# Kernel tuning notes

Hardware: AMD Instinct MI355X
Metric: run time of the kernel (lower is better)

## Reference

```python
import jax, jax.numpy as jnp
import numpy as np

K = 3          # kernel_size (forced by hardcoded padding=1 in query unfold)
PAD = 1        # padding
C_IN = 64      # conv in_channels (x has C_IN + 5 channels)
C_OUT = 128    # out_channels
B, H, W = 16, 32, 32


def unfold(x, k, pad=0, mode='constant'):
    """torch.nn.functional.unfold equivalent. x: (B,C,H,W) -> (B, C*k*k, L).
    Ordering matches torch: channel slowest, then kernel row, then kernel col."""
    if pad:
        x = jnp.pad(x, ((0, 0), (0, 0), (pad, pad), (pad, pad)), mode=mode)
    b, c, h, w = x.shape
    oh, ow = h - k + 1, w - k + 1
    # (B, C, k*k, oh, ow) with patch index i*k+j
    patches = jnp.stack([x[:, :, i:i + oh, j:j + ow]
                         for i in range(k) for j in range(k)], axis=2)
    return patches.reshape(b, c * k * k, oh * ow)


def conv2d(x, w, b, pad):
    out = jax.lax.conv_general_dilated(
        x, w, window_strides=(1, 1), padding=[(pad, pad), (pad, pad)],
        dimension_numbers=('NCHW', 'OIHW', 'NCHW'))
    return out + b[None, :, None, None]


def setup_inputs() -> dict:
    key = jax.random.key(0)
    ks = jax.random.split(key, 6)
    fan1 = C_IN * K * K
    fan2 = C_OUT * 1 * 1
    return {
        'x': jax.random.normal(ks[0], (B, C_IN + 5, H, W), jnp.float32),
        'conv_w': jax.random.normal(ks[1], (C_OUT, C_IN, K, K), jnp.float32) / np.sqrt(fan1),
        'conv_b': jax.random.normal(ks[2], (C_OUT,), jnp.float32) * 0.01,
        'conv2_w': jax.random.normal(ks[3], (1, C_OUT, 1, 1), jnp.float32) / np.sqrt(fan2),
        'conv2_b': jax.random.normal(ks[4], (1,), jnp.float32) * 0.01,
        'shapes_kernel': jax.random.uniform(ks[5], (1, C_OUT, K * K * 5, 1), jnp.float32),
    }


def reference(x, conv_w, conv_b, conv2_w, conv2_b, shapes_kernel):
    k, pad = K, PAD
    center = k * k // 2

    conv_out = conv2d(x[:, :-5], conv_w, conv_b, pad)          # (B, C_OUT, H', W')
    b, cout, oh, ow = conv_out.shape
    L = oh * ow

    # shape-channel windows (replication-padded), center-relative positions
    sw = unfold(x[:, -5:], k, pad, 'edge').reshape(b, 5, k * k, L)
    sw = sw.at[:, 0:2].add(-sw[:, 0:2, center:center + 1])

    # L1 distance of each window to each learned shape kernel
    sd = jnp.abs(sw.reshape(b, 1, 5 * k * k, L) - shapes_kernel).sum(axis=2)  # (B, C_OUT, L)
    sd = sd.reshape(b, cout, oh, ow)

    saf = jax.nn.relu(conv_out / (sd + 1.0))                    # shape_attended_features

    q = conv2d(saf, conv2_w, conv2_b, 0) / jnp.sqrt(jnp.float32(cout))  # (B, 1, H', W')
    qu = jax.nn.softmax(unfold(q, k, 1), axis=1)[:, None]       # (B, 1, k*k, L), zero-padded

    u_mean = unfold(x[:, -5:-3], k, pad, 'edge').reshape(b, 2, k * k, L)
    means = (u_mean * qu).sum(axis=2)                           # (B, 2, L)

    v1 = (unfold(x[:, -3:-1], k, pad, 'edge').reshape(b, 2, k * k, L) * qu).sum(axis=2)
    v2 = (((u_mean - means[:, :, None, :]) ** 2) * qu).sum(axis=2)
    var = v1 + v2                                               # (B, 2, L)

    c1 = (unfold(x[:, -1:], k, pad, 'edge').reshape(b, 1, k * k, L) * qu).sum(axis=2)
    c2 = ((u_mean[:, 0:1] - means[:, 0:1, None, :]) *
          (u_mean[:, 1:2] - means[:, 1:2, None, :]) * qu).sum(axis=2)
    covar = c1 + c2                                             # (B, 1, L)

    agg = jnp.concatenate([means, var, covar], axis=1).reshape(b, 5, oh, ow)
    return jnp.concatenate([saf, agg], axis=1)                  # (B, C_OUT+5, H', W')
```

## Files before the change

### kernel.cpp

```cpp
#include <hip/hip_runtime.h>
#include <math.h>

#define CI 64
#define CO 128
#define CX 69
#define LPIX 1024

typedef __attribute__((ext_vector_type(8))) short bf16x8;
typedef __attribute__((ext_vector_type(4))) float f32x4;

#define WMF_OFF  0
#define SKT_OFF  147456
#define QP_OFF   (147456 + 23040)

__device__ __forceinline__ unsigned short f2bf(float f) {
  unsigned u = __float_as_uint(f);
  unsigned r = (u + 0x7fffu + ((u >> 16) & 1u)) >> 16;
  return (unsigned short)r;
}

__launch_bounds__(256)
__global__ void prepW(const float* __restrict__ cwg,
                      const float* __restrict__ skg,
                      unsigned short* __restrict__ wmf,
                      float* __restrict__ skt) {
  int i = blockIdx.x * 256 + threadIdx.x;
  if (i < 128 * 9 * 64) {
    int co = i / 576, rem = i - co * 576;
    int tap = rem >> 6, ci = rem & 63;
    wmf[i] = f2bf(cwg[co * 576 + ci * 9 + tap]);
  } else {
    int d = i - 128 * 9 * 64;
    if (d < 45 * 128) {
      int j = d >> 7, co = d & 127;
      skt[j * 128 + co] = skg[co * 45 + j];
    }
  }
}

__launch_bounds__(256, 2)
__global__ void convFused(const float* __restrict__ xg,
                          const unsigned short* __restrict__ wmfg,
                          const float* __restrict__ cbg,
                          const float* __restrict__ w2g,
                          const float* __restrict__ sktg,
                          float* __restrict__ qp,
                          float* __restrict__ outg) {
  __shared__ char arena[18432];
  __shared__ float lds_sx[5 * 144];
  __shared__ float qred[4][64];

  unsigned short* ldsB = (unsigned short*)arena;
  float* lds_c = (float*)arena;

  const int tid = threadIdx.x;
  const int blk = blockIdx.x;
  const int coh = blk & 1;
  const int rp  = (blk >> 1) & 15;
  const int b   = blk >> 5;
  const int r0  = rp * 2;

  const int w    = tid >> 6;
  const int lane = tid & 63;
  const int rsel = w >> 1;
  const int cq   = w & 1;
  const int n16  = lane & 15;
  const int kq   = lane >> 4;

  const float* xb = xg + (size_t)b * CX * LPIX;
  const float* xs = xb + CI * LPIX;

  {
    const int col = tid & 31;
    const int grp = tid >> 5;
    const int slot = col + 1;
    const int swk = (slot & 7) << 3;
    #pragma unroll
    for (int it = 0; it < 16; ++it) {
      const int rc  = grp + it * 8;
      const int row = rc >> 5;
      const int ci  = (rc & 31) * 2;
      const int grow = r0 - 1 + row;
      unsigned v = 0;
      if ((unsigned)grow < 32u) {
        float f0 = xb[ci * LPIX + grow * 32 + col];
        float f1 = xb[(ci + 1) * LPIX + grow * 32 + col];
        v = (unsigned)f2bf(f0) | ((unsigned)f2bf(f1) << 16);
      }
      const int gslot = ((ci >> 3) << 3) ^ swk;
      ((unsigned*)ldsB)[(((row * 36 + slot) << 6) + gslot + (ci & 7)) >> 1] = v;
    }
    for (int idx = tid; idx < 512; idx += 256) {
      const int row = idx >> 7;
      const int s4  = (idx >> 5) & 3;
      const int sl  = (s4 == 0) ? 0 : (32 + s4);
      const int ci  = (idx & 31) * 2;
      const int gsl = ((ci >> 3) << 3) ^ ((sl & 7) << 3);
      ((unsigned*)ldsB)[(((row * 36 + sl) << 6) + gsl + (ci & 7)) >> 1] = 0;
    }
  }

  for (int idx = tid; idx < 5 * 144; idx += 256) {
    int c = idx / 144, rem = idx - c * 144;
    int s = rem / 36, j = rem - s * 36;
    int hh = r0 - 1 + s; hh = hh < 0 ? 0 : (hh > 31 ? 31 : hh);
    int col = j - 1;     col = col < 0 ? 0 : (col > 31 ? 31 : col);
    lds_sx[idx] = xs[c * LPIX + hh * 32 + col];
  }
  __syncthreads();

  const unsigned short* ap[2][2];
  #pragma unroll
  for (int ch = 0; ch < 2; ++ch)
    #pragma unroll
    for (int ct = 0; ct < 2; ++ct)
      ap[ch][ct] = wmfg + (size_t)(coh * 64 + cq * 32 + ct * 16 + n16) * 576
                   + ch * 32 + kq * 8;

  f32x4 acc[2][2] = {};

  #pragma unroll
  for (int tap = 0; tap < 9; ++tap) {
    const int dr = tap / 3, dc = tap % 3;
    const int rowst = rsel + dr;
    #pragma unroll
    for (int ch = 0; ch < 2; ++ch) {
      const int g = (ch << 2) + kq;
      bf16x8 bfr[2];
      #pragma unroll
      for (int t = 0; t < 2; ++t) {
        const int slot = t * 16 + n16 + dc;
        const int gs = (g ^ (slot & 7)) << 3;
        bfr[t] = *(const bf16x8*)(ldsB + ((rowst * 36 + slot) << 6) + gs);
      }
      #pragma unroll
      for (int ct = 0; ct < 2; ++ct) {
        bf16x8 a = *(const bf16x8*)(ap[ch][ct] + tap * 64);
        acc[0][ct] = __builtin_amdgcn_mfma_f32_16x16x32_bf16(a, bfr[0], acc[0][ct], 0, 0, 0);
        acc[1][ct] = __builtin_amdgcn_mfma_f32_16x16x32_bf16(a, bfr[1], acc[1][ct], 0, 0, 0);
      }
    }
  }
  __syncthreads();

  #pragma unroll
  for (int pt = 0; pt < 2; ++pt) {
    const int pxl = rsel * 32 + pt * 16 + n16;
    #pragma unroll
    for (int ct = 0; ct < 2; ++ct) {
      const int cog = cq * 8 + ct * 4 + kq;
      const int sg  = cog ^ (pxl & 7);
      *(f32x4*)&lds_c[pxl * 64 + sg * 4] = acc[pt][ct];
    }
  }
  __syncthreads();

  const int wS   = __builtin_amdgcn_readfirstlane(w);
  const int co0g = coh * 64 + wS * 16;
  const int pxl  = lane;

  float cvals[16];
  #pragma unroll
  for (int g = 0; g < 4; ++g) {
    const int cog = wS * 4 + g;
    const int sg  = cog ^ (pxl & 7);
    *(f32x4*)&cvals[g * 4] = *(const f32x4*)&lds_c[pxl * 64 + sg * 4];
  }

  const int xbase = (pxl >> 5) * 36 + (pxl & 31);
  float swv[45];
  {
    const float c0 = lds_sx[0 * 144 + 37 + xbase];
    const float c1 = lds_sx[1 * 144 + 37 + xbase];
    #pragma unroll
    for (int c = 0; c < 5; ++c) {
      float ctr = (c == 0) ? c0 : ((c == 1) ? c1 : 0.f);
      #pragma unroll
      for (int s = 0; s < 3; ++s)
        #pragma unroll
        for (int dc = 0; dc < 3; ++dc)
          swv[c * 9 + s * 3 + dc] = lds_sx[c * 144 + s * 36 + dc + xbase] - ctr;
    }
  }

  float sd[16];
  #pragma unroll
  for (int k = 0; k < 16; ++k) sd[k] = 0.f;
  const float* skt = sktg + co0g;
  #pragma unroll
  for (int j = 0; j < 45; ++j) {
    const float sv = swv[j];
    #pragma unroll
    for (int k = 0; k < 16; ++k)
      sd[k] += fabsf(sv - skt[j * 128 + k]);
  }

  float qpv = 0.f;
  float* ob = outg + ((size_t)b * 133 + co0g) * LPIX + (r0 + (pxl >> 5)) * 32 + (pxl & 31);
  #pragma unroll
  for (int k = 0; k < 16; ++k) {
    float v = (cvals[k] + cbg[co0g + k]) * __builtin_amdgcn_rcpf(sd[k] + 1.0f);
    v = v > 0.f ? v : 0.f;
    ob[(size_t)k * LPIX] = v;
    qpv = fmaf(v, w2g[co0g + k], qpv);
  }

  qred[w][lane] = qpv;
  __syncthreads();
  if (tid < 64) {
    float q = qred[0][tid] + qred[1][tid] + qred[2][tid] + qred[3][tid];
    qp[coh * 16384 + b * LPIX + r0 * 32 + tid] = q;
  }
}

__launch_bounds__(64)
__global__ void statsB(const float* __restrict__ xg,
                       const float* __restrict__ qp,
                       const float* __restrict__ b2g,
                       float* __restrict__ outg) {
  const int gid = blockIdx.x * 64 + threadIdx.x;
  const int b = gid >> 10;
  const int h = (gid >> 5) & 31;
  const int w = gid & 31;

  const float b2 = b2g[0];
  const float* q0 = qp + (size_t)b * LPIX;
  float qv[9];
  float m = -1e30f;
  #pragma unroll
  for (int t = 0; t < 9; ++t) {
    int hh = h + t / 3 - 1, wc = w + t % 3 - 1;
    float v = 0.f;
    if ((unsigned)hh < 32u && (unsigned)wc < 32u) {
      int off = hh * 32 + wc;
      v = (q0[off] + q0[16384 + off] + b2) * 0.08838834764831845f;
    }
    qv[t] = v;
    m = fmaxf(m, v);
  }
  float ssum = 0.f;
  #pragma unroll
  for (int t = 0; t < 9; ++t) { qv[t] = expf(qv[t] - m); ssum += qv[t]; }
  const float inv = 1.f / ssum;

  const float* xs = xg + ((size_t)b * CX + CI) * LPIX;
  float um0[9], um1[9];
  float m0 = 0.f, m1 = 0.f, v1a = 0.f, v1b = 0.f, c1 = 0.f;
  #pragma unroll
  for (int t = 0; t < 9; ++t) {
    int hh = h + t / 3 - 1; hh = hh < 0 ? 0 : (hh > 31 ? 31 : hh);
    int wc = w + t % 3 - 1; wc = wc < 0 ? 0 : (wc > 31 ? 31 : wc);
    int off = hh * 32 + wc;
    float quv = qv[t] * inv;
    qv[t] = quv;
    float a0 = xs[off];
    float a1 = xs[LPIX + off];
    float b0 = xs[2 * LPIX + off];
    float b1 = xs[3 * LPIX + off];
    float cc = xs[4 * LPIX + off];
    um0[t] = a0; um1[t] = a1;
    m0 = fmaf(a0, quv, m0);
    m1 = fmaf(a1, quv, m1);
    v1a = fmaf(b0, quv, v1a);
    v1b = fmaf(b1, quv, v1b);
    c1 = fmaf(cc, quv, c1);
  }
  float var0 = v1a, var1 = v1b, cov = c1;
  #pragma unroll
  for (int t = 0; t < 9; ++t) {
    float d0 = um0[t] - m0, d1 = um1[t] - m1;
    var0 = fmaf(d0 * d0, qv[t], var0);
    var1 = fmaf(d1 * d1, qv[t], var1);
    cov  = fmaf(d0 * d1, qv[t], cov);
  }
  float* ob = outg + ((size_t)b * 133 + 128) * LPIX + h * 32 + w;
  ob[0 * LPIX] = m0;
  ob[1 * LPIX] = m1;
  ob[2 * LPIX] = var0;
  ob[3 * LPIX] = var1;
  ob[4 * LPIX] = cov;
}

extern "C" void kernel_launch(void* const* d_in, const int* in_sizes, int n_in,
                              void* d_out, int out_size, void* d_ws, size_t ws_size,
                              hipStream_t stream) {
  const float* x  = (const float*)d_in[0];
  const float* cw = (const float*)d_in[1];
  const float* cb = (const float*)d_in[2];
  const float* w2 = (const float*)d_in[3];
  const float* b2 = (const float*)d_in[4];
  const float* sk = (const float*)d_in[5];
  float* out = (float*)d_out;

  unsigned short* wmf = (unsigned short*)((char*)d_ws + WMF_OFF);
  float* skt = (float*)((char*)d_ws + SKT_OFF);
  float* qp  = (float*)((char*)d_ws + QP_OFF);

  prepW<<<dim3(311), dim3(256), 0, stream>>>(cw, sk, wmf, skt);
  convFused<<<dim3(512), dim3(256), 0, stream>>>(x, wmf, cb, w2, skt, qp, out);
  statsB<<<dim3(256), dim3(64), 0, stream>>>(x, qp, b2, out);
}
```

Before: 36.95 us.

## Double convFused block to 512 threads, preload weights in registers, vectorize input staging

The fused conv kernel now runs 8 waves per block instead of 4. Each wave owns one 16-channel output tile per row and preloads all 18 bf16 weight fragments into registers before the MFMA loop. Input staging switches from scalar to float4 global loads, with one pass per thread. The epilogue handles 8 channels per wave instead of 16, which spreads the L1-distance and ReLU work across more waves. In exchange it uses more registers per thread and changes occupancy under launch_bounds(512,4).

```diff
diff --git a/kernel.cpp b/kernel.cpp
--- a/kernel.cpp
+++ b/kernel.cpp
@@ -38,7 +38,7 @@
   }
 }
 
-__launch_bounds__(256, 2)
+__launch_bounds__(512, 4)
 __global__ void convFused(const float* __restrict__ xg,
                           const unsigned short* __restrict__ wmfg,
                           const float* __restrict__ cbg,
@@ -48,7 +48,7 @@
                           float* __restrict__ outg) {
   __shared__ char arena[18432];
   __shared__ float lds_sx[5 * 144];
-  __shared__ float qred[4][64];
+  __shared__ float qred[8][64];
 
   unsigned short* ldsB = (unsigned short*)arena;
   float* lds_c = (float*)arena;
@@ -62,45 +62,58 @@
 
   const int w    = tid >> 6;
   const int lane = tid & 63;
-  const int rsel = w >> 1;
-  const int cq   = w & 1;
+  const int rsel = w >> 2;
+  const int ct   = w & 3;
   const int n16  = lane & 15;
   const int kq   = lane >> 4;
 
   const float* xb = xg + (size_t)b * CX * LPIX;
   const float* xs = xb + CI * LPIX;
 
+  bf16x8 areg[2][9];
   {
-    const int col = tid & 31;
-    const int grp = tid >> 5;
-    const int slot = col + 1;
-    const int swk = (slot & 7) << 3;
-    #pragma unroll
-    for (int it = 0; it < 16; ++it) {
-      const int rc  = grp + it * 8;
-      const int row = rc >> 5;
-      const int ci  = (rc & 31) * 2;
-      const int grow = r0 - 1 + row;
-      unsigned v = 0;
-      if ((unsigned)grow < 32u) {
-        float f0 = xb[ci * LPIX + grow * 32 + col];
-        float f1 = xb[(ci + 1) * LPIX + grow * 32 + col];
-        v = (unsigned)f2bf(f0) | ((unsigned)f2bf(f1) << 16);
-      }
-      const int gslot = ((ci >> 3) << 3) ^ swk;
+    const unsigned short* abase =
+        wmfg + (size_t)(coh * 64 + ct * 16 + n16) * 576 + kq * 8;
+    #pragma unroll
+    for (int ch = 0; ch < 2; ++ch)
+      #pragma unroll
+      for (int tap = 0; tap < 9; ++tap)
+        areg[ch][tap] = *(const bf16x8*)(abase + tap * 64 + ch * 32);
+  }
+
+  {
+    const int row  = tid >> 7;
+    const int cip  = (tid >> 2) & 31;
+    const int colq = tid & 3;
+    const int ci   = cip * 2;
+    const int c0   = colq * 8;
+    const int grow = r0 - 1 + row;
+    f32x4 u0a = {}, u0b = {}, u1a = {}, u1b = {};
+    if ((unsigned)grow < 32u) {
+      const float* p0 = xb + ci * LPIX + grow * 32 + c0;
+      u0a = *(const f32x4*)p0;          u0b = *(const f32x4*)(p0 + 4);
+      u1a = *(const f32x4*)(p0 + LPIX); u1b = *(const f32x4*)(p0 + LPIX + 4);
+    }
+    #pragma unroll
+    for (int cc = 0; cc < 8; ++cc) {
+      float f0 = (cc < 4) ? u0a[cc] : u0b[cc - 4];
+      float f1 = (cc < 4) ? u1a[cc] : u1b[cc - 4];
+      unsigned v = (unsigned)f2bf(f0) | ((unsigned)f2bf(f1) << 16);
+      const int slot  = c0 + cc + 1;
+      const int gslot = ((ci >> 3) << 3) ^ ((slot & 7) << 3);
       ((unsigned*)ldsB)[(((row * 36 + slot) << 6) + gslot + (ci & 7)) >> 1] = v;
     }
-    for (int idx = tid; idx < 512; idx += 256) {
-      const int row = idx >> 7;
-      const int s4  = (idx >> 5) & 3;
+    {
+      const int prw = tid >> 7;
+      const int s4  = (tid >> 5) & 3;
       const int sl  = (s4 == 0) ? 0 : (32 + s4);
-      const int ci  = (idx & 31) * 2;
-      const int gsl = ((ci >> 3) << 3) ^ ((sl & 7) << 3);
-      ((unsigned*)ldsB)[(((row * 36 + sl) << 6) + gsl + (ci & 7)) >> 1] = 0;
-    }
-  }
-
-  for (int idx = tid; idx < 5 * 144; idx += 256) {
+      const int ci2 = (tid & 31) * 2;
+      const int gsl = ((ci2 >> 3) << 3) ^ ((sl & 7) << 3);
+      ((unsigned*)ldsB)[(((prw * 36 + sl) << 6) + gsl + (ci2 & 7)) >> 1] = 0;
+    }
+  }
+
+  for (int idx = tid; idx < 5 * 144; idx += 512) {
     int c = idx / 144, rem = idx - c * 144;
     int s = rem / 36, j = rem - s * 36;
     int hh = r0 - 1 + s; hh = hh < 0 ? 0 : (hh > 31 ? 31 : hh);
@@ -109,16 +122,7 @@
   }
   __syncthreads();
 
-  const unsigned short* ap[2][2];
-  #pragma unroll
-  for (int ch = 0; ch < 2; ++ch)
-    #pragma unroll
-    for (int ct = 0; ct < 2; ++ct)
-      ap[ch][ct] = wmfg + (size_t)(coh * 64 + cq * 32 + ct * 16 + n16) * 576
-                   + ch * 32 + kq * 8;
-
-  f32x4 acc[2][2] = {};
-
+  f32x4 acc[2] = {};
   #pragma unroll
   for (int tap = 0; tap < 9; ++tap) {
     const int dr = tap / 3, dc = tap % 3;
@@ -126,18 +130,13 @@
     #pragma unroll
     for (int ch = 0; ch < 2; ++ch) {
       const int g = (ch << 2) + kq;
-      bf16x8 bfr[2];
       #pragma unroll
-      for (int t = 0; t < 2; ++t) {
-        const int slot = t * 16 + n16 + dc;
+      for (int pt = 0; pt < 2; ++pt) {
+        const int slot = pt * 16 + n16 + dc;
         const int gs = (g ^ (slot & 7)) << 3;
-        bfr[t] = *(const bf16x8*)(ldsB + ((rowst * 36 + slot) << 6) + gs);
-      }
-      #pragma unroll
-      for (int ct = 0; ct < 2; ++ct) {
-        bf16x8 a = *(const bf16x8*)(ap[ch][ct] + tap * 64);
-        acc[0][ct] = __builtin_amdgcn_mfma_f32_16x16x32_bf16(a, bfr[0], acc[0][ct], 0, 0, 0);
-        acc[1][ct] = __builtin_amdgcn_mfma_f32_16x16x32_bf16(a, bfr[1], acc[1][ct], 0, 0, 0);
+        bf16x8 bfr = *(const bf16x8*)(ldsB + ((rowst * 36 + slot) << 6) + gs);
+        acc[pt] = __builtin_amdgcn_mfma_f32_16x16x32_bf16(areg[ch][tap], bfr,
+                                                          acc[pt], 0, 0, 0);
       }
     }
   }
@@ -146,23 +145,20 @@
   #pragma unroll
   for (int pt = 0; pt < 2; ++pt) {
     const int pxl = rsel * 32 + pt * 16 + n16;
-    #pragma unroll
-    for (int ct = 0; ct < 2; ++ct) {
-      const int cog = cq * 8 + ct * 4 + kq;
-      const int sg  = cog ^ (pxl & 7);
-      *(f32x4*)&lds_c[pxl * 64 + sg * 4] = acc[pt][ct];
-    }
+    const int cog = ct * 4 + kq;
+    const int sg  = cog ^ (pxl & 7);
+    *(f32x4*)&lds_c[pxl * 64 + sg * 4] = acc[pt];
   }
   __syncthreads();
 
   const int wS   = __builtin_amdgcn_readfirstlane(w);
-  const int co0g = coh * 64 + wS * 16;
+  const int co0g = coh * 64 + wS * 8;
   const int pxl  = lane;
 
-  float cvals[16];
-  #pragma unroll
-  for (int g = 0; g < 4; ++g) {
-    const int cog = wS * 4 + g;
+  float cvals[8];
+  #pragma unroll
+  for (int g = 0; g < 2; ++g) {
+    const int cog = wS * 2 + g;
     const int sg  = cog ^ (pxl & 7);
     *(f32x4*)&cvals[g * 4] = *(const f32x4*)&lds_c[pxl * 64 + sg * 4];
   }
@@ -183,22 +179,22 @@
     }
   }
 
-  float sd[16];
-  #pragma unroll
-  for (int k = 0; k < 16; ++k) sd[k] = 0.f;
+  float sd[8];
+  #pragma unroll
+  for (int k = 0; k < 8; ++k) sd[k] = 0.f;
   const float* skt = sktg + co0g;
   #pragma unroll
   for (int j = 0; j < 45; ++j) {
     const float sv = swv[j];
     #pragma unroll
-    for (int k = 0; k < 16; ++k)
+    for (int k = 0; k < 8; ++k)
       sd[k] += fabsf(sv - skt[j * 128 + k]);
   }
 
   float qpv = 0.f;
   float* ob = outg + ((size_t)b * 133 + co0g) * LPIX + (r0 + (pxl >> 5)) * 32 + (pxl & 31);
   #pragma unroll
-  for (int k = 0; k < 16; ++k) {
+  for (int k = 0; k < 8; ++k) {
     float v = (cvals[k] + cbg[co0g + k]) * __builtin_amdgcn_rcpf(sd[k] + 1.0f);
     v = v > 0.f ? v : 0.f;
     ob[(size_t)k * LPIX] = v;
@@ -208,7 +204,9 @@
   qred[w][lane] = qpv;
   __syncthreads();
   if (tid < 64) {
-    float q = qred[0][tid] + qred[1][tid] + qred[2][tid] + qred[3][tid];
+    float q = 0.f;
+    #pragma unroll
+    for (int w8 = 0; w8 < 8; ++w8) q += qred[w8][tid];
     qp[coh * 16384 + b * LPIX + r0 * 32 + tid] = q;
   }
 }
@@ -297,6 +295,6 @@
   float* qp  = (float*)((char*)d_ws + QP_OFF);
 
   prepW<<<dim3(311), dim3(256), 0, stream>>>(cw, sk, wmf, skt);
-  convFused<<<dim3(512), dim3(256), 0, stream>>>(x, wmf, cb, w2, skt, qp, out);
+  convFused<<<dim3(512), dim3(512), 0, stream>>>(x, wmf, cb, w2, skt, qp, out);
   statsB<<<dim3(256), dim3(64), 0, stream>>>(x, qp, b2, out);
 }
```

Measured after the change: 32.42 us. 1.14x faster.
